# Optimization experiments

Hardware: AMD Instinct MI355X
Metric: run time of the kernel (lower is better)

## Reference

```python
import jax, jax.numpy as jnp
import numpy as np

N = 25000   # total nodes across the batch of graphs
K = 16      # sample_size_per_layer
H = 128     # encoder_hidden_dim
E = 128     # embedding_size
V = 32000   # vocab size
B = 50      # number of graphs / sql sequences
L = 128     # sql sequence length
NT = 4      # tokens per node name
NLAYERS = 3 # sample_layer_size


def _nrm(k, shape):
    return jax.random.normal(k, shape, dtype=jnp.float32) * 0.05


def setup_inputs() -> dict:
    key = jax.random.key(0)
    ks = iter(jax.random.split(key, 48))
    inp = {}
    inp["embed"] = _nrm(next(ks), (V, E))
    for d in ("seq_f", "seq_b", "node"):
        inp[d + "_Wih"] = _nrm(next(ks), (4 * H, E))
        inp[d + "_Whh"] = _nrm(next(ks), (4 * H, H))
        inp[d + "_b"] = _nrm(next(ks), (4 * H,))
    for d in ("fw", "bw"):
        inp[d + "_att0"] = _nrm(next(ks), (2, H))
        inp[d + "_attr"] = _nrm(next(ks), (NLAYERS - 1, 2, 2 * H))
        inp[d + "_Wg0"] = _nrm(next(ks), (H, H))
        inp[d + "_bg0"] = _nrm(next(ks), (H,))
        inp[d + "_Wgr"] = _nrm(next(ks), (NLAYERS - 1, 2 * H, 2 * H))
        inp[d + "_bgr"] = _nrm(next(ks), (NLAYERS - 1, 2 * H))
        inp[d + "_Wo0"] = _nrm(next(ks), (2, H, H))
        inp[d + "_bo0"] = _nrm(next(ks), (2, H))
        inp[d + "_Wor"] = _nrm(next(ks), (NLAYERS - 1, 2, 2 * H, H))
        inp[d + "_bor"] = _nrm(next(ks), (NLAYERS - 1, 2, H))
    inp["node_features"] = jax.random.randint(next(ks), (N, NT), 0, V)
    inp["fw_adj"] = jax.random.randint(next(ks), (N + 1, K), 0, N + 1)  # index N = zero-pad row
    inp["bw_adj"] = jax.random.randint(next(ks), (N + 1, K), 0, N + 1)
    inp["idx_sql_seqs"] = jax.random.randint(next(ks), (B, L), 0, V)
    lens = jax.random.randint(next(ks), (B,), 16, L + 1)
    inp["sql_seqs_lens"] = lens.at[0].set(L)  # ensure max(lens) == L like pad_packed
    inp["max_len"] = 1000  # nodes per graph (equal-size graphs)
    return inp


def _lstm(x, Wih, Whh, b):
    # x: [B, T, E] -> [B, T, H]; torch LSTM gate order i, f, g, o (bih+bhh folded into b)
    xg = jnp.einsum('bte,ge->btg', x, Wih) + b
    h0 = jnp.zeros((x.shape[0], Whh.shape[1]), x.dtype)
    def step(carry, gt):
        h, c = carry
        g = gt + h @ Whh.T
        i, f, gg, o = jnp.split(g, 4, axis=-1)
        c = jax.nn.sigmoid(f) * c + jax.nn.sigmoid(i) * jnp.tanh(gg)
        h = jax.nn.sigmoid(o) * jnp.tanh(c)
        return (h, c), h
    _, hs = jax.lax.scan(step, (h0, h0), jnp.swapaxes(xg, 0, 1))
    return jnp.swapaxes(hs, 0, 1)


def _gated_attn(self_h, neigh, att, Wg, bg, Wo, bo):
    # additive attention over K sampled neighbors, gated context, concat output (2*H)
    scores = jnp.einsum('nkd,d->nk', neigh, att[1]) + (self_h @ att[0])[:, None]
    a = jax.nn.softmax(scores, axis=-1)
    ctx = jnp.einsum('nk,nkd->nd', a, neigh)
    gate = jax.nn.sigmoid(self_h @ Wg + bg)
    from_self = jax.nn.relu(self_h @ Wo[0] + bo[0])
    from_neigh = jax.nn.relu((gate * ctx) @ Wo[1] + bo[1])
    return jnp.concatenate([from_self, from_neigh], axis=-1)


def reference(embed, seq_f_Wih, seq_f_Whh, seq_f_b, seq_b_Wih, seq_b_Whh, seq_b_b,
              node_Wih, node_Whh, node_b,
              fw_att0, fw_attr, fw_Wg0, fw_bg0, fw_Wgr, fw_bgr, fw_Wo0, fw_bo0, fw_Wor, fw_bor,
              bw_att0, bw_attr, bw_Wg0, bw_bg0, bw_Wgr, bw_bgr, bw_Wo0, bw_bo0, bw_Wor, bw_bor,
              node_features, fw_adj, bw_adj, idx_sql_seqs, sql_seqs_lens, max_len):
    Bq, Lq = idx_sql_seqs.shape
    # --- SQL sequence encoder: bi-LSTM with length-aware reverse (pack/pad semantics) ---
    se = embed[idx_sql_seqs]                              # [B, L, E]
    fwd = _lstm(se, seq_f_Wih, seq_f_Whh, seq_f_b)
    rev_idx = jnp.clip(sql_seqs_lens[:, None] - 1 - jnp.arange(Lq)[None, :], 0, Lq - 1)
    se_rev = jnp.take_along_axis(se, rev_idx[..., None], 1)
    bwd = jnp.take_along_axis(_lstm(se_rev, seq_b_Wih, seq_b_Whh, seq_b_b), rev_idx[..., None], 1)
    valid = (jnp.arange(Lq)[None, :] < sql_seqs_lens[:, None])[..., None]
    seqs_encoding = jnp.concatenate([fwd, bwd], -1) * valid  # padded positions zeroed
    seqs_encoding_mask = (idx_sql_seqs == 0)
    # --- node feature encoder: last hidden of a uni-LSTM over node tokens ---
    node_embedding = _lstm(embed[node_features], node_Wih, node_Whh, node_b)[:, -1, :]  # [N, H]
    fw_nbrs = fw_adj[:-1]  # [N, K]
    bw_nbrs = bw_adj[:-1]
    fw_hidden = node_embedding
    bw_hidden = node_embedding
    for l in range(NLAYERS):
        pad = jnp.zeros((1, fw_hidden.shape[1]), fw_hidden.dtype)
        fn = jnp.concatenate([fw_hidden, pad], 0)[fw_nbrs]  # [N, K, d]
        if l == 0:
            fw_hidden = _gated_attn(fw_hidden, fn, fw_att0, fw_Wg0, fw_bg0, fw_Wo0, fw_bo0)
        else:
            j = l - 1
            fw_hidden = _gated_attn(fw_hidden, fn, fw_attr[j], fw_Wgr[j], fw_bgr[j], fw_Wor[j], fw_bor[j])
        bn_ = jnp.concatenate([bw_hidden, pad], 0)[bw_nbrs]
        if l == 0:
            bw_hidden = _gated_attn(bw_hidden, bn_, bw_att0, bw_Wg0, bw_bg0, bw_Wo0, bw_bo0)
        else:
            j = l - 1
            bw_hidden = _gated_attn(bw_hidden, bn_, bw_attr[j], bw_Wgr[j], bw_bgr[j], bw_Wor[j], bw_bor[j])
    hidden = jax.nn.relu(jnp.concatenate([fw_hidden, bw_hidden], -1))  # [N, 4H]
    graph_hidden = hidden.reshape(hidden.shape[0] // max_len, max_len, hidden.shape[1])
    graph_embedding = graph_hidden.max(axis=1)
    return (graph_hidden, graph_embedding, max_len, seqs_encoding, seqs_encoding_mask)
```

## Files before the change

kernel.cpp:

```cpp
#include <hip/hip_runtime.h>
#include <math.h>

#define NN 25000
#define KNB 16
#define HH 128
#define VV 32000
#define BB 50
#define LL 128
#define NTK 4
#define NGRAPH 25
#define GCH 20

typedef __attribute__((ext_vector_type(8))) short s16x8;
typedef __attribute__((ext_vector_type(4))) float f32x4;
typedef _Float16 h16x2 __attribute__((ext_vector_type(2)));

__device__ __forceinline__ float fexp2(float x) {
#if __has_builtin(__builtin_amdgcn_exp2f)
    return __builtin_amdgcn_exp2f(x);
#else
    return exp2f(x);
#endif
}
__device__ __forceinline__ float frcp(float x) {
#if __has_builtin(__builtin_amdgcn_rcpf)
    return __builtin_amdgcn_rcpf(x);
#else
    return 1.f / x;
#endif
}
__device__ __forceinline__ float fsigm(float x) { return frcp(1.f + fexp2(x * -1.4426950408889634f)); }
__device__ __forceinline__ float ftanh(float x) { return 1.f - 2.f * frcp(1.f + fexp2(x * 2.8853900817779268f)); }

__device__ __forceinline__ unsigned short f2bf(float x) {
    unsigned int u = __float_as_uint(x);
    unsigned int r = (u + 0x7fffu + ((u >> 16) & 1u)) >> 16;
    return (unsigned short)r;
}
__device__ __forceinline__ float bf2f(unsigned int b) {
    return __uint_as_float((b & 0xffffu) << 16);
}

template<int CTRL>
__device__ __forceinline__ float qxor(float x) {
#if __has_builtin(__builtin_amdgcn_mov_dpp)
    return __int_as_float(__builtin_amdgcn_mov_dpp(__float_as_int(x), CTRL, 0xf, 0xf, true));
#else
    int m = (CTRL == 0xB1) ? 1 : (CTRL == 0x4E) ? 2 : 3;
    return __shfl_xor(x, m, 64);
#endif
}

__device__ __forceinline__ float hdot(unsigned int a, unsigned int b, float c) {
#if __has_builtin(__builtin_amdgcn_fdot2)
    return __builtin_amdgcn_fdot2(__builtin_bit_cast(h16x2, a), __builtin_bit_cast(h16x2, b), c, false);
#else
    h16x2 av = __builtin_bit_cast(h16x2, a), bv = __builtin_bit_cast(h16x2, b);
    return c + (float)av[0] * (float)bv[0] + (float)av[1] * (float)bv[1];
#endif
}

__global__ __launch_bounds__(256) void embconv_k(const float* __restrict__ e,
                                                 unsigned short* __restrict__ o)
{
    int i = blockIdx.x * 256 + threadIdx.x;
    if (i < VV * 128) o[i] = f2bf(e[i]);
}

__global__ __launch_bounds__(256) void wprep_k(
    const float* __restrict__ ndWih, const float* __restrict__ ndWhh,
    const float* __restrict__ fWg0, const float* __restrict__ fWgr,
    const float* __restrict__ fWo0, const float* __restrict__ fWor,
    const float* __restrict__ bWg0, const float* __restrict__ bWgr,
    const float* __restrict__ bWo0, const float* __restrict__ bWor,
    const float* __restrict__ sfWih, const float* __restrict__ sbWih,
    const float* __restrict__ sfWhh, const float* __restrict__ sbWhh,
    unsigned short* __restrict__ dst)
{
    int idx = blockIdx.x * 256 + threadIdx.x;
    if (idx >= 1146880) return;
    if (idx >= 884736) {
        int r = idx - 884736;
        int d = r >> 17;
        int o = r & 131071;
        int pairIdx = o >> 1, hf = o & 1;
        int k2 = pairIdx >> 9, n = pairIdx & 511;
        int k = k2 * 2 + hf;
        int unit = n >> 2, gate = n & 3;
        const float* W = d ? sbWhh : sfWhh;
        _Float16 hv = (_Float16)W[(gate * 128 + unit) * 128 + k];
        dst[idx] = __builtin_bit_cast(unsigned short, hv);
        return;
    }
    float val;
    if (idx < 131072) {
        int r = idx >> 8, k = idx & 255;
        int unit = r >> 2, gate = r & 3;
        int srow = (gate << 7) + unit;
        val = (k < 128) ? ndWih[srow * 128 + k] : ndWhh[srow * 128 + (k - 128)];
    } else if (idx < 753664) {
        int r = idx - 131072;
        int dir = r / 311296;
        int o = r % 311296;
        const float* Wg0 = dir ? bWg0 : fWg0;
        const float* Wgr = dir ? bWgr : fWgr;
        const float* Wo0 = dir ? bWo0 : fWo0;
        const float* Wor = dir ? bWor : fWor;
        if (o < 16384) {
            int n = o >> 7, k = o & 127;
            val = Wg0[k * 128 + n];
        } else if (o < 147456) {
            int p = o - 16384;
            int j = p >> 16, q = p & 65535;
            int n = q >> 8, k = q & 255;
            val = Wgr[j * 65536 + k * 256 + n];
        } else if (o < 180224) {
            int p = o - 147456;
            int s = p >> 14, q = p & 16383;
            int n = q >> 7, k = q & 127;
            val = Wo0[s * 16384 + k * 128 + n];
        } else {
            int p = o - 180224;
            int js = p >> 15, q = p & 32767;
            int n = q >> 8, k = q & 255;
            val = Wor[js * 32768 + k * 128 + n];
        }
    } else if (idx < 819200) {
        val = sfWih[idx - 753664];
    } else {
        val = sbWih[idx - 819200];
    }
    dst[idx] = f2bf(val);
}

__global__ __launch_bounds__(256) void tokrev_k(const int* __restrict__ idx,
                                                const int* __restrict__ lens,
                                                int* __restrict__ tokrev)
{
    int t = blockIdx.x * 256 + threadIdx.x;
    if (t >= BB * LL) return;
    int b = t / LL, tt = t % LL;
    int r = lens[b] - 1 - tt;
    r = r < 0 ? 0 : (r > LL - 1 ? LL - 1 : r);
    tokrev[t] = idx[b * LL + r];
}

__global__ __launch_bounds__(256) void hgemm1_k(
    const unsigned short* __restrict__ embedbf,
    const int* __restrict__ gidxA, const int* __restrict__ gidxB,
    const unsigned short* __restrict__ WtA, const unsigned short* __restrict__ WtB,
    const float* __restrict__ biasA, const float* __restrict__ biasB,
    float* __restrict__ outA, float* __restrict__ outB)
{
    __shared__ unsigned short Asm[128 * 64];
    __shared__ unsigned short Bsm[128 * 64];
    const int tid = threadIdx.x;
    const int lane = tid & 63, w = tid >> 6;
    const int wm = w >> 1, wn = w & 1;
    const int lane15 = lane & 15, hi = lane >> 4;
    const int y = blockIdx.y;
    const int* gidx = (y < 4) ? gidxA : gidxB;
    const unsigned short* Wt = (y < 4) ? WtA : WtB;
    const float* bias = (y < 4) ? biasA : biasB;
    float* outp = (y < 4) ? outA : outB;
    const int bm0 = blockIdx.x * 128, bn0 = (y & 3) * 128;
    const int M = BB * LL, K = 128;
    f32x4 acc[4][4];
#pragma unroll
    for (int i = 0; i < 4; ++i)
#pragma unroll
        for (int j = 0; j < 4; ++j) acc[i][j] = (f32x4){0.f, 0.f, 0.f, 0.f};

    for (int kt = 0; kt < K; kt += 64) {
#pragma unroll
        for (int r = 0; r < 4; ++r) {
            int id = tid + r * 256;
            int row = id >> 3, cc = id & 7;
            int m = bm0 + row;
            s16x8 v = {0, 0, 0, 0, 0, 0, 0, 0};
            if (m < M) {
                int g = gidx[m];
                v = *(const s16x8*)(embedbf + (size_t)g * 128 + kt + cc * 8);
            }
            int byt = (cc * 16) ^ ((row & 7) << 4);
            *(s16x8*)((char*)Asm + row * 128 + byt) = v;
        }
#pragma unroll
        for (int r = 0; r < 4; ++r) {
            int id = tid + r * 256;
            int row = id >> 3, cc = id & 7;
            s16x8 v = *(const s16x8*)(Wt + (size_t)(bn0 + row) * K + kt + cc * 8);
            int byt = (cc * 16) ^ ((row & 7) << 4);
            *(s16x8*)((char*)Bsm + row * 128 + byt) = v;
        }
        __syncthreads();
#pragma unroll
        for (int ks = 0; ks < 2; ++ks) {
            s16x8 af[4], bf[4];
#pragma unroll
            for (int mi = 0; mi < 4; ++mi) {
                int row = wm * 64 + mi * 16 + lane15;
                int byt = (ks * 64 + (hi * 16)) ^ ((row & 7) << 4);
                af[mi] = *(const s16x8*)((char*)Asm + row * 128 + byt);
            }
#pragma unroll
            for (int ni = 0; ni < 4; ++ni) {
                int row = wn * 64 + ni * 16 + lane15;
                int byt = (ks * 64 + (hi * 16)) ^ ((row & 7) << 4);
                bf[ni] = *(const s16x8*)((char*)Bsm + row * 128 + byt);
            }
#pragma unroll
            for (int mi = 0; mi < 4; ++mi)
#pragma unroll
                for (int ni = 0; ni < 4; ++ni)
                    acc[mi][ni] = __builtin_amdgcn_mfma_f32_16x16x32_bf16(af[mi], bf[ni], acc[mi][ni], 0, 0, 0);
        }
        __syncthreads();
    }
#pragma unroll
    for (int mi = 0; mi < 4; ++mi) {
#pragma unroll
        for (int ni = 0; ni < 4; ++ni) {
            int n = bn0 + wn * 64 + ni * 16 + lane15;
#pragma unroll
            for (int j = 0; j < 4; ++j) {
                int m = bm0 + wm * 64 + mi * 16 + hi * 4 + j;
                if (m < M) {
                    float v = acc[mi][ni][j] + bias[n];
                    int nn = ((n & 127) << 2) | (n >> 7);
                    outp[(size_t)m * 512 + nn] = v;
                }
            }
        }
    }
}

__global__ __launch_bounds__(512, 4) void node_seq_k(
    const unsigned short* __restrict__ embedbf,
    const int* __restrict__ nodefeat,
    const unsigned short* __restrict__ hrd,
    const unsigned short* __restrict__ nodeW,
    const float* __restrict__ ndb,
    unsigned short* __restrict__ hwr,
    unsigned short* __restrict__ cbuf,
    int step,
    const float* __restrict__ xgf, const float* __restrict__ xgb,
    const unsigned short* __restrict__ wseq,
    const int* __restrict__ lens,
    float* __restrict__ senc,
    unsigned short* __restrict__ hseq, float* __restrict__ cseq)
{
    __shared__ __align__(16) unsigned char smem[32768 + 512];
    const int bid = blockIdx.x;
    const int tid = threadIdx.x;

    if (bid >= 784) {
        int sid = bid - 784;
        int dir = sid >= BB ? 1 : 0;
        int b = dir ? sid - BB : sid;
        int len = lens[b];
        int t0 = step * 32;
        if (t0 >= len) return;
        int t1 = t0 + 32 < len ? t0 + 32 : len;
        const float* xg = (dir ? xgb : xgf) + (size_t)b * LL * 512;
        const unsigned int* wp = (const unsigned int*)(wseq + dir * 131072);
        int q = tid & 3, unit = tid >> 2;
        unsigned int wreg[64];
#pragma unroll
        for (int k2 = 0; k2 < 64; ++k2) wreg[k2] = wp[k2 * 512 + tid];
        unsigned short* hlsq = (unsigned short*)smem;
        float cj = 0.f;
        if (step == 0) {
            if (tid < 128) hlsq[tid] = 0;
        } else {
            if (tid < 128) hlsq[tid] = hseq[sid * 128 + tid];
            if (q == 0) cj = cseq[sid * 128 + unit];
        }
        __syncthreads();
        float xcur = xg[(size_t)t0 * 512 + tid];
        int pb = 0;
        for (int t = t0; t < t1; ++t) {
            float xnext = (t + 1 < t1) ? xg[(size_t)(t + 1) * 512 + tid] : 0.f;
            const uint4* hp = (const uint4*)&hlsq[pb * 128];
            float p0 = 0.f, p1 = 0.f, p2 = 0.f, p3 = 0.f;
#pragma unroll
            for (int i = 0; i < 4; ++i) {
                uint4 h0 = hp[i * 4 + 0], h1 = hp[i * 4 + 1], h2 = hp[i * 4 + 2], h3 = hp[i * 4 + 3];
                const unsigned int* w0 = &wreg[i * 16];
                p0 = hdot(h0.x, w0[0], p0);  p0 = hdot(h0.y, w0[1], p0);
                p0 = hdot(h0.z, w0[2], p0);  p0 = hdot(h0.w, w0[3], p0);
                p1 = hdot(h1.x, w0[4], p1);  p1 = hdot(h1.y, w0[5], p1);
                p1 = hdot(h1.z, w0[6], p1);  p1 = hdot(h1.w, w0[7], p1);
                p2 = hdot(h2.x, w0[8], p2);  p2 = hdot(h2.y, w0[9], p2);
                p2 = hdot(h2.z, w0[10], p2); p2 = hdot(h2.w, w0[11], p2);
                p3 = hdot(h3.x, w0[12], p3); p3 = hdot(h3.y, w0[13], p3);
                p3 = hdot(h3.z, w0[14], p3); p3 = hdot(h3.w, w0[15], p3);
            }
            float accv = xcur + ((p0 + p1) + (p2 + p3));
            float tv = (q == 2) ? ftanh(accv) : fsigm(accv);
            float v1 = __shfl_xor(tv, 1), v2 = __shfl_xor(tv, 2), v3 = __shfl_xor(tv, 3);
            if (q == 0) {
                cj = v1 * cj + tv * v2;
                float hv = v3 * ftanh(cj);
                _Float16 hh = (_Float16)hv;
                hlsq[(pb ^ 1) * 128 + unit] = __builtin_bit_cast(unsigned short, hh);
                int tout = dir ? (len - 1 - t) : t;
                senc[((size_t)b * LL + tout) * 256 + dir * 128 + unit] = hv;
            }
            __syncthreads();
            pb ^= 1;
            xcur = xnext;
        }
        if (q == 0) cseq[sid * 128 + unit] = cj;
        if (tid < 128) hseq[sid * 128 + tid] = hlsq[pb * 128 + tid];
        return;
    }

    unsigned short* Asm = (unsigned short*)smem;
    unsigned short* Bsm = (unsigned short*)(smem + 16384);
    const int lane = tid & 63, w = tid >> 6;
    const int wm = w & 1, wn = w >> 1;
    const int lane15 = lane & 15, hi = lane >> 4, q = lane & 3;
    const int bx = bid % 196, y = bid / 196;
    const int bm0 = bx * 128, bn0 = y * 128;
    const int czero = (step == 0);

    f32x4 acc[4][2];
#pragma unroll
    for (int i = 0; i < 4; ++i)
#pragma unroll
        for (int j = 0; j < 2; ++j) acc[i][j] = (f32x4){0.f, 0.f, 0.f, 0.f};

    for (int kt = 0; kt < 256; kt += 64) {
#pragma unroll
        for (int r = 0; r < 2; ++r) {
            int id = tid + r * 512;
            int row = id >> 3, cc = id & 7;
            int m = bm0 + row;
            s16x8 v = {0, 0, 0, 0, 0, 0, 0, 0};
            if (m < NN) {
                int k0 = kt + cc * 8;
                if (k0 < 128) {
                    int g = nodefeat[m * NTK + step];
                    v = *(const s16x8*)(embedbf + (size_t)g * 128 + k0);
                } else if (!czero) {
                    v = *(const s16x8*)(hrd + (size_t)m * 128 + (k0 - 128));
                }
            }
            int byt = (cc * 16) ^ ((row & 7) << 4);
            *(s16x8*)((char*)Asm + row * 128 + byt) = v;
        }
#pragma unroll
        for (int r = 0; r < 2; ++r) {
            int id = tid + r * 512;
            int row = id >> 3, cc = id & 7;
            s16x8 v = *(const s16x8*)(nodeW + (size_t)(bn0 + row) * 256 + kt + cc * 8);
            int byt = (cc * 16) ^ ((row & 7) << 4);
            *(s16x8*)((char*)Bsm + row * 128 + byt) = v;
        }
        __syncthreads();
#pragma unroll
        for (int ks = 0; ks < 2; ++ks) {
            s16x8 af[4], bf[2];
#pragma unroll
            for (int mi = 0; mi < 4; ++mi) {
                int row = wm * 64 + mi * 16 + lane15;
                int byt = (ks * 64 + (hi * 16)) ^ ((row & 7) << 4);
                af[mi] = *(const s16x8*)((char*)Asm + row * 128 + byt);
            }
#pragma unroll
            for (int ni = 0; ni < 2; ++ni) {
                int row = wn * 32 + ni * 16 + lane15;
                int byt = (ks * 64 + (hi * 16)) ^ ((row & 7) << 4);
                bf[ni] = *(const s16x8*)((char*)Bsm + row * 128 + byt);
            }
#pragma unroll
            for (int mi = 0; mi < 4; ++mi)
#pragma unroll
                for (int ni = 0; ni < 2; ++ni)
                    acc[mi][ni] = __builtin_amdgcn_mfma_f32_16x16x32_bf16(af[mi], bf[ni], acc[mi][ni], 0, 0, 0);
        }
        __syncthreads();
    }
    unsigned short* cb = cbuf + (((size_t)bid * 8 + w) * 64 + lane) * 8;
    float crv[8];
    if (czero) {
#pragma unroll
        for (int i = 0; i < 8; ++i) crv[i] = 0.f;
    } else {
        uint4 w0 = *(const uint4*)cb;
        unsigned int wd[4] = {w0.x, w0.y, w0.z, w0.w};
#pragma unroll
        for (int i = 0; i < 8; ++i) crv[i] = bf2f(wd[i >> 1] >> ((i & 1) * 16));
    }
    const bool qb0 = (lane & 1), qb1 = (lane & 2);
#pragma unroll
    for (int mi = 0; mi < 4; ++mi) {
#pragma unroll
        for (int ni = 0; ni < 2; ++ni) {
            int n = bn0 + wn * 32 + ni * 16 + lane15;
            int unit = n >> 2;
            float bval = ndb[((n & 3) << 7) + unit];
#pragma unroll
            for (int j = 0; j < 4; ++j) {
                float v = acc[mi][ni][j] + bval;
                float tv = (q == 2) ? ftanh(v) : fsigm(v);
                float v1 = qxor<0xB1>(tv), v2 = qxor<0x4E>(tv), v3 = qxor<0x1B>(tv);
                if (q == j) {
                    float gf = qb0 ? (qb1 ? v2 : tv) : (qb1 ? v3 : v1);
                    float gig = qb0 ? (v1 * v3) : (tv * v2);
                    float go = qb0 ? (qb1 ? tv : v2) : (qb1 ? v1 : v3);
                    float cc = gf * crv[mi * 2 + ni] + gig;
                    crv[mi * 2 + ni] = cc;
                    int m = bm0 + wm * 64 + mi * 16 + hi * 4 + j;
                    if (m < NN) hwr[(size_t)m * HH + unit] = f2bf(go * ftanh(cc));
                }
            }
        }
    }
    unsigned int wd[4];
#pragma unroll
    for (int p = 0; p < 4; ++p)
        wd[p] = (unsigned int)f2bf(crv[2 * p]) | ((unsigned int)f2bf(crv[2 * p + 1]) << 16);
    *(uint4*)cb = make_uint4(wd[0], wd[1], wd[2], wd[3]);
}

template<int OF32OUT>
__global__ __launch_bounds__(256) void hgemm3b_k(
    const unsigned short* __restrict__ cur, int curds,
    unsigned short* __restrict__ ctx, int ctxds,
    const unsigned short* __restrict__ wg, int wgds,
    const float* __restrict__ bgf, const float* __restrict__ bgb,
    const unsigned short* __restrict__ wo, int wods, int wrs,
    const float* __restrict__ bof, const float* __restrict__ bob,
    void* __restrict__ outb, int outds, int ocolDS,
    int M, int K, int D, int gatetiles, int roleoff)
{
    __shared__ unsigned short Asm[128 * 64];
    __shared__ unsigned short Bsm[128 * 64];
    const int tid = threadIdx.x;
    const int lane = tid & 63, w = tid >> 6;
    const int wm = w >> 1, wn = w & 1;
    const int bm0 = blockIdx.x * 128;
    const int dir = blockIdx.z, y = blockIdx.y;
    const bool isgate = y < gatetiles;
    const int r = isgate ? 0 : (y - gatetiles + roleoff);
    const int colBase = isgate ? y * 128 : r * 128;
    unsigned short* ctxd = ctx + (size_t)dir * ctxds;
    const unsigned short* A = (isgate || r == 0) ? (cur + (size_t)dir * curds) : ctxd;
    const unsigned short* Wt = isgate ? (wg + (size_t)dir * wgds + (size_t)colBase * K)
                                      : (wo + (size_t)dir * wods + (size_t)r * wrs);
    const float* bias = (isgate ? (dir ? bgb : bgf) : (dir ? bob : bof)) + colBase;

    f32x4 acc[4][4];
#pragma unroll
    for (int i = 0; i < 4; ++i)
#pragma unroll
        for (int j = 0; j < 4; ++j) acc[i][j] = (f32x4){0.f, 0.f, 0.f, 0.f};

    for (int kt = 0; kt < K; kt += 64) {
#pragma unroll
        for (int rr = 0; rr < 4; ++rr) {
            int id = tid + rr * 256;
            int row = id >> 3, cc = id & 7;
            int m = bm0 + row;
            s16x8 v = {0, 0, 0, 0, 0, 0, 0, 0};
            if (m < M) v = *(const s16x8*)(A + (size_t)m * K + kt + cc * 8);
            int byt = (cc * 16) ^ ((row & 7) << 4);
            *(s16x8*)((char*)Asm + row * 128 + byt) = v;
        }
#pragma unroll
        for (int rr = 0; rr < 4; ++rr) {
            int id = tid + rr * 256;
            int row = id >> 3, cc = id & 7;
            s16x8 v = *(const s16x8*)(Wt + (size_t)row * K + kt + cc * 8);
            int byt = (cc * 16) ^ ((row & 7) << 4);
            *(s16x8*)((char*)Bsm + row * 128 + byt) = v;
        }
        __syncthreads();
#pragma unroll
        for (int ks = 0; ks < 2; ++ks) {
            s16x8 af[4], bf[4];
#pragma unroll
            for (int mi = 0; mi < 4; ++mi) {
                int row = wm * 64 + mi * 16 + (lane & 15);
                int byt = (ks * 64 + ((lane >> 4) * 16)) ^ ((row & 7) << 4);
                af[mi] = *(const s16x8*)((char*)Asm + row * 128 + byt);
            }
#pragma unroll
            for (int ni = 0; ni < 4; ++ni) {
                int row = wn * 64 + ni * 16 + (lane & 15);
                int byt = (ks * 64 + ((lane >> 4) * 16)) ^ ((row & 7) << 4);
                bf[ni] = *(const s16x8*)((char*)Bsm + row * 128 + byt);
            }
#pragma unroll
            for (int mi = 0; mi < 4; ++mi)
#pragma unroll
                for (int ni = 0; ni < 4; ++ni)
                    acc[mi][ni] = __builtin_amdgcn_mfma_f32_16x16x32_bf16(af[mi], bf[ni], acc[mi][ni], 0, 0, 0);
        }
        __syncthreads();
    }
#pragma unroll
    for (int mi = 0; mi < 4; ++mi) {
#pragma unroll
        for (int ni = 0; ni < 4; ++ni) {
            int ncol = wn * 64 + ni * 16 + (lane & 15);
            int col = colBase + ncol;
#pragma unroll
            for (int j = 0; j < 4; ++j) {
                int m = bm0 + wm * 64 + mi * 16 + (lane >> 4) * 4 + j;
                if (m < M) {
                    float v = acc[mi][ni][j] + bias[ncol];
                    if (isgate) {
                        v = fsigm(v) * bf2f(ctxd[(size_t)m * D + col]);
                        ctxd[(size_t)m * D + col] = f2bf(v);
                    } else if (OF32OUT) {
                        v = fmaxf(v, 0.f);
                        ((float*)outb)[(size_t)m * 512 + dir * ocolDS + col] = v;
                    } else {
                        v = fmaxf(v, 0.f);
                        ((unsigned short*)outb)[(size_t)dir * outds + (size_t)m * 256 + col] = f2bf(v);
                    }
                }
            }
        }
    }
}

__global__ __launch_bounds__(256) void finalize_k(const int* __restrict__ idx,
                                                  const int* __restrict__ lens,
                                                  float* __restrict__ senc,
                                                  float* __restrict__ mask,
                                                  float* __restrict__ omax,
                                                  const int* __restrict__ mlin)
{
    int id = blockIdx.x * 256 + threadIdx.x;
    if (id == 0) omax[0] = (float)mlin[0];
    if (id >= BB * LL * 64) return;
    int row = id >> 6, c = id & 63;
    int b = row / LL, tt = row % LL;
    if (c == 0) mask[row] = (idx[row] == 0) ? 1.f : 0.f;
    if (tt >= lens[b]) *(float4*)&senc[(size_t)row * 256 + c * 4] = make_float4(0.f, 0.f, 0.f, 0.f);
}

template<int D>
__global__ __launch_bounds__(256) void sdot_k(const unsigned short* __restrict__ hidb, int hidds,
                                              const float* __restrict__ a1f, const float* __restrict__ a1b,
                                              float* __restrict__ s1)
{
    constexpr int V = D / 64;
    int dir = blockIdx.y;
    const unsigned short* hid = hidb + (size_t)dir * hidds;
    const float* att1 = dir ? a1b : a1f;
    int lane = threadIdx.x & 63, wid = threadIdx.x >> 6;
    int n = blockIdx.x * 4 + wid;
    if (n >= NN) return;
    float p = 0.f;
    if (V == 2) {
        unsigned int u = *(const unsigned int*)(hid + (size_t)n * D + lane * 2);
        p = bf2f(u) * att1[lane * 2] + bf2f(u >> 16) * att1[lane * 2 + 1];
    } else {
        uint2 u = *(const uint2*)(hid + (size_t)n * D + lane * 4);
        p = bf2f(u.x) * att1[lane * 4] + bf2f(u.x >> 16) * att1[lane * 4 + 1]
          + bf2f(u.y) * att1[lane * 4 + 2] + bf2f(u.y >> 16) * att1[lane * 4 + 3];
    }
#pragma unroll
    for (int m = 1; m < 64; m <<= 1) p += __shfl_xor(p, m);
    if (lane == 0) s1[dir * NN + n] = p;
}

template<int D>
__global__ __launch_bounds__(256) void attn_ctx3_k(const unsigned short* __restrict__ hidb, int hidds,
                                                   const int* __restrict__ adj0, const int* __restrict__ adj1,
                                                   const float* __restrict__ s1,
                                                   unsigned short* __restrict__ ctxb, int ctxds)
{
    constexpr int V = D / 64;
    int dir = blockIdx.y;
    const unsigned short* hid = hidb + (size_t)dir * hidds;
    const int* adj = dir ? adj1 : adj0;
    unsigned short* ctx = ctxb + (size_t)dir * ctxds;
    int lane = threadIdx.x & 63, wid = threadIdx.x >> 6;
    int n = blockIdx.x * 4 + wid;
    if (n >= NN) return;
    int nb[KNB];
    float sc[KNB];
#pragma unroll
    for (int k = 0; k < KNB; ++k) nb[k] = adj[n * KNB + k];
#pragma unroll
    for (int k = 0; k < KNB; ++k) sc[k] = (nb[k] < NN) ? s1[dir * NN + nb[k]] : 0.f;
    float mx = sc[0];
#pragma unroll
    for (int k = 1; k < KNB; ++k) mx = fmaxf(mx, sc[k]);
    float s = 0.f;
#pragma unroll
    for (int k = 0; k < KNB; ++k) { sc[k] = fexp2((sc[k] - mx) * 1.4426950408889634f); s += sc[k]; }
    float inv = frcp(s);
    float accv[V];
#pragma unroll
    for (int j = 0; j < V; ++j) accv[j] = 0.f;
#pragma unroll
    for (int k = 0; k < KNB; ++k) {
        if (nb[k] < NN) {
            if (V == 2) {
                unsigned int u = *(const unsigned int*)(hid + (size_t)nb[k] * D + lane * 2);
                accv[0] += sc[k] * bf2f(u);
                accv[1] += sc[k] * bf2f(u >> 16);
            } else {
                uint2 u = *(const uint2*)(hid + (size_t)nb[k] * D + lane * 4);
                accv[0] += sc[k] * bf2f(u.x);
                accv[1] += sc[k] * bf2f(u.x >> 16);
                accv[2] += sc[k] * bf2f(u.y);
                accv[3] += sc[k] * bf2f(u.y >> 16);
            }
        }
    }
#pragma unroll
    for (int j2 = 0; j2 < V; j2 += 2) {
        unsigned int pk = (unsigned int)f2bf(accv[j2] * inv) | ((unsigned int)f2bf(accv[j2 + 1] * inv) << 16);
        *(unsigned int*)(ctx + (size_t)n * D + lane * V + j2) = pk;
    }
}

__global__ __launch_bounds__(512) void gmax1_k(const float* __restrict__ gh, float* __restrict__ part)
{
    int g = blockIdx.x, ch = blockIdx.y;
    int c = threadIdx.x;
    const float* p = gh + ((size_t)g * 1000 + ch * (1000 / GCH)) * 512 + c;
    float m = -1e30f;
#pragma unroll 5
    for (int i = 0; i < 1000 / GCH; ++i) m = fmaxf(m, p[(size_t)i * 512]);
    part[((size_t)g * GCH + ch) * 512 + c] = m;
}

__global__ __launch_bounds__(512) void gmax2_k(const float* __restrict__ part, float* __restrict__ ge)
{
    int g = blockIdx.x;
    int c = threadIdx.x;
    float m = -1e30f;
#pragma unroll
    for (int i = 0; i < GCH; ++i) m = fmaxf(m, part[((size_t)g * GCH + i) * 512 + c]);
    ge[g * 512 + c] = m;
}

extern "C" void kernel_launch(void* const* d_in, const int* in_sizes, int n_in,
                              void* d_out, int out_size, void* d_ws, size_t ws_size,
                              hipStream_t stream)
{
    const float* embed = (const float*)d_in[0];
    const float* sfWhh = (const float*)d_in[2];
    const float* sfb   = (const float*)d_in[3];
    const float* sbWhh = (const float*)d_in[5];
    const float* sbb   = (const float*)d_in[6];
    const float* ndWih = (const float*)d_in[7];
    const float* ndWhh = (const float*)d_in[8];
    const float* ndb   = (const float*)d_in[9];
    const int* nodefeat = (const int*)d_in[30];
    const int* adj0     = (const int*)d_in[31];
    const int* adj1     = (const int*)d_in[32];
    const int* idxseq   = (const int*)d_in[33];
    const int* lens     = (const int*)d_in[34];
    const int* mlin     = (const int*)d_in[35];

    float* ws = (float*)d_ws;
    unsigned short* warena  = (unsigned short*)ws;
    unsigned short* embedbf = (unsigned short*)(ws + 573440);
    float* xgf = ws + 2621440;
    float* xgb = ws + 5898240;
    int*   tokrev = (int*)(ws + 9175040);
    unsigned short* hbf  = (unsigned short*)(ws + 9181440);
    unsigned short* hbf2 = (unsigned short*)(ws + 10781440);
    unsigned short* cbuf = (unsigned short*)(ws + 12381440);
    unsigned short* HA   = (unsigned short*)(ws + 573440);
    unsigned short* HB   = (unsigned short*)(ws + 6973440);
    unsigned short* ctxb = (unsigned short*)(ws + 13987072);
    float* s1buf = ws + 20387072;
    unsigned short* hseq = (unsigned short*)(ws + 20437072);
    float* cseq = ws + 20449872;
    float* gmaxp = ws + 573440;

    float* outf  = (float*)d_out;
    float* gh    = outf;
    float* ge    = outf + 12800000;
    float* omax  = outf + 12812800;
    float* senc  = outf + 12812801;
    float* omask = outf + 14451201;

    tokrev_k<<<dim3((BB * LL + 255) / 256), dim3(256), 0, stream>>>(idxseq, lens, tokrev);
    embconv_k<<<dim3(VV * 128 / 256), dim3(256), 0, stream>>>(embed, embedbf);
    wprep_k<<<dim3(4480), dim3(256), 0, stream>>>(ndWih, ndWhh,
        (const float*)d_in[12], (const float*)d_in[14], (const float*)d_in[16], (const float*)d_in[18],
        (const float*)d_in[22], (const float*)d_in[24], (const float*)d_in[26], (const float*)d_in[28],
        (const float*)d_in[1], (const float*)d_in[4], sfWhh, sbWhh, warena);

    hgemm1_k<<<dim3(50, 8), dim3(256), 0, stream>>>(embedbf, idxseq, tokrev,
        warena + 753664, warena + 819200, sfb, sbb, xgf, xgb);

    for (int t = 0; t < NTK; ++t) {
        const unsigned short* hrd = (t & 1) ? hbf2 : hbf;
        unsigned short* hwr = (t & 1) ? hbf : hbf2;
        node_seq_k<<<dim3(884), dim3(512), 0, stream>>>(embedbf, nodefeat, hrd,
            warena, ndb, hwr, cbuf, t,
            xgf, xgb, warena + 884736, lens, senc, hseq, cseq);
    }
    finalize_k<<<dim3(1600), dim3(256), 0, stream>>>(idxseq, lens, senc, omask, omax, mlin);

    for (int l = 0; l < 3; ++l) {
        int D = (l == 0) ? 128 : 256;
        int j = l - 1;
        const unsigned short* curb = (l == 0) ? hbf : (l == 1 ? HA : HB);
        int curds = (l == 0) ? 0 : NN * 256;
        int ctxds = NN * D;
        const float* a1f = (l == 0) ? (const float*)d_in[10] + 128 : (const float*)d_in[11] + (size_t)j * 512 + 256;
        const float* a1b = (l == 0) ? (const float*)d_in[20] + 128 : (const float*)d_in[21] + (size_t)j * 512 + 256;

        if (D == 128) {
            sdot_k<128><<<dim3(NN / 4, 2), dim3(256), 0, stream>>>(curb, curds, a1f, a1b, s1buf);
            attn_ctx3_k<128><<<dim3(NN / 4, 2), dim3(256), 0, stream>>>(curb, curds, adj0, adj1, s1buf, ctxb, ctxds);
        } else {
            sdot_k<256><<<dim3(NN / 4, 2), dim3(256), 0, stream>>>(curb, curds, a1f, a1b, s1buf);
            attn_ctx3_k<256><<<dim3(NN / 4, 2), dim3(256), 0, stream>>>(curb, curds, adj0, adj1, s1buf, ctxb, ctxds);
        }

        const unsigned short* wgb = warena + 131072 + ((l == 0) ? 0 : 16384 + j * 65536);
        const float* bgf = (l == 0) ? (const float*)d_in[13] : (const float*)d_in[15] + (size_t)j * 256;
        const float* bgb = (l == 0) ? (const float*)d_in[23] : (const float*)d_in[25] + (size_t)j * 256;
        const unsigned short* wob = warena + 131072 + ((l == 0) ? 147456 : 180224 + j * 65536);
        int wrs = (l == 0) ? 16384 : 32768;
        const float* bof = (l == 0) ? (const float*)d_in[17] : (const float*)d_in[19] + (size_t)j * 256;
        const float* bob = (l == 0) ? (const float*)d_in[27] : (const float*)d_in[29] + (size_t)j * 256;
        int gt = D / 128;
        void* ob = (l == 2) ? (void*)gh : (void*)((l == 0) ? HA : HB);
        int outds = NN * 256;

        if (l == 2) {
            hgemm3b_k<1><<<dim3(196, gt + 1, 2), dim3(256), 0, stream>>>(curb, curds, ctxb, ctxds,
                wgb, 311296, bgf, bgb, wob, 311296, wrs, bof, bob, ob, 0, 256, NN, D, D, gt, 0);
            hgemm3b_k<1><<<dim3(196, 1, 2), dim3(256), 0, stream>>>(curb, curds, ctxb, ctxds,
                wgb, 311296, bgf, bgb, wob, 311296, wrs, bof, bob, ob, 0, 256, NN, D, D, 0, 1);
        } else {
            hgemm3b_k<0><<<dim3(196, gt + 1, 2), dim3(256), 0, stream>>>(curb, curds, ctxb, ctxds,
                wgb, 311296, bgf, bgb, wob, 311296, wrs, bof, bob, ob, outds, 0, NN, D, D, gt, 0);
            hgemm3b_k<0><<<dim3(196, 1, 2), dim3(256), 0, stream>>>(curb, curds, ctxb, ctxds,
                wgb, 311296, bgf, bgb, wob, 311296, wrs, bof, bob, ob, outds, 0, NN, D, D, 0, 1);
        }
    }

    gmax1_k<<<dim3(NGRAPH, GCH), dim3(512), 0, stream>>>(gh, gmaxp);
    gmax2_k<<<dim3(NGRAPH), dim3(512), 0, stream>>>(gmaxp, ge);
}
```

Baseline: 653.9 us.

## Fuse gate and output GEMMs per layer into one kernel keeping activations in LDS

Replaces the two hgemm3b launches per layer with a single layer_fused_k kernel. Each block loads its 128-row tile of the current hidden state into shared memory once, computes the gate GEMMs and writes the gated context into shared memory instead of global, then runs both output GEMMs from LDS. This removes the global round trip for the gated context, the repeated A-tile loads and one launch per layer, and swizzles the block index so the two directions are spread across the grid. In exchange it uses large LDS allocations (up to about 144KB at D=256) with one 512-thread block per CU, which limits occupancy, and the grid is only 392 blocks.

Result: faster. 606.2 us (median of 5 runs) (-7.3%).

```diff
diff --git a/kernel.cpp b/kernel.cpp
--- a/kernel.cpp
+++ b/kernel.cpp
@@ -425,102 +425,166 @@
     *(uint4*)cb = make_uint4(wd[0], wd[1], wd[2], wd[3]);
 }
 
-template<int OF32OUT>
-__global__ __launch_bounds__(256) void hgemm3b_k(
+template<int D, int OF32OUT>
+__global__ __launch_bounds__(512, 1) void layer_fused_k(
     const unsigned short* __restrict__ cur, int curds,
-    unsigned short* __restrict__ ctx, int ctxds,
+    const unsigned short* __restrict__ ctx, int ctxds,
     const unsigned short* __restrict__ wg, int wgds,
     const float* __restrict__ bgf, const float* __restrict__ bgb,
     const unsigned short* __restrict__ wo, int wods, int wrs,
     const float* __restrict__ bof, const float* __restrict__ bob,
-    void* __restrict__ outb, int outds, int ocolDS,
-    int M, int K, int D, int gatetiles, int roleoff)
-{
-    __shared__ unsigned short Asm[128 * 64];
-    __shared__ unsigned short Bsm[128 * 64];
+    void* __restrict__ outb, int outds)
+{
+    __shared__ unsigned short As[128 * D];
+    __shared__ unsigned short Gs[128 * D];
+    __shared__ unsigned short Ws[128 * 64];
+    constexpr int gt = D / 128;
     const int tid = threadIdx.x;
     const int lane = tid & 63, w = tid >> 6;
-    const int wm = w >> 1, wn = w & 1;
-    const int bm0 = blockIdx.x * 128;
-    const int dir = blockIdx.z, y = blockIdx.y;
-    const bool isgate = y < gatetiles;
-    const int r = isgate ? 0 : (y - gatetiles + roleoff);
-    const int colBase = isgate ? y * 128 : r * 128;
-    unsigned short* ctxd = ctx + (size_t)dir * ctxds;
-    const unsigned short* A = (isgate || r == 0) ? (cur + (size_t)dir * curds) : ctxd;
-    const unsigned short* Wt = isgate ? (wg + (size_t)dir * wgds + (size_t)colBase * K)
-                                      : (wo + (size_t)dir * wods + (size_t)r * wrs);
-    const float* bias = (isgate ? (dir ? bgb : bgf) : (dir ? bob : bof)) + colBase;
-
-    f32x4 acc[4][4];
-#pragma unroll
-    for (int i = 0; i < 4; ++i)
-#pragma unroll
-        for (int j = 0; j < 4; ++j) acc[i][j] = (f32x4){0.f, 0.f, 0.f, 0.f};
-
-    for (int kt = 0; kt < K; kt += 64) {
-#pragma unroll
-        for (int rr = 0; rr < 4; ++rr) {
-            int id = tid + rr * 256;
-            int row = id >> 3, cc = id & 7;
-            int m = bm0 + row;
-            s16x8 v = {0, 0, 0, 0, 0, 0, 0, 0};
-            if (m < M) v = *(const s16x8*)(A + (size_t)m * K + kt + cc * 8);
-            int byt = (cc * 16) ^ ((row & 7) << 4);
-            *(s16x8*)((char*)Asm + row * 128 + byt) = v;
-        }
-#pragma unroll
-        for (int rr = 0; rr < 4; ++rr) {
-            int id = tid + rr * 256;
-            int row = id >> 3, cc = id & 7;
-            s16x8 v = *(const s16x8*)(Wt + (size_t)row * K + kt + cc * 8);
-            int byt = (cc * 16) ^ ((row & 7) << 4);
-            *(s16x8*)((char*)Bsm + row * 128 + byt) = v;
-        }
-        __syncthreads();
-#pragma unroll
-        for (int ks = 0; ks < 2; ++ks) {
-            s16x8 af[4], bf[4];
-#pragma unroll
-            for (int mi = 0; mi < 4; ++mi) {
-                int row = wm * 64 + mi * 16 + (lane & 15);
-                int byt = (ks * 64 + ((lane >> 4) * 16)) ^ ((row & 7) << 4);
-                af[mi] = *(const s16x8*)((char*)Asm + row * 128 + byt);
-            }
-#pragma unroll
-            for (int ni = 0; ni < 4; ++ni) {
-                int row = wn * 64 + ni * 16 + (lane & 15);
-                int byt = (ks * 64 + ((lane >> 4) * 16)) ^ ((row & 7) << 4);
-                bf[ni] = *(const s16x8*)((char*)Bsm + row * 128 + byt);
-            }
-#pragma unroll
-            for (int mi = 0; mi < 4; ++mi)
-#pragma unroll
-                for (int ni = 0; ni < 4; ++ni)
-                    acc[mi][ni] = __builtin_amdgcn_mfma_f32_16x16x32_bf16(af[mi], bf[ni], acc[mi][ni], 0, 0, 0);
-        }
-        __syncthreads();
-    }
-#pragma unroll
-    for (int mi = 0; mi < 4; ++mi) {
-#pragma unroll
-        for (int ni = 0; ni < 4; ++ni) {
-            int ncol = wn * 64 + ni * 16 + (lane & 15);
-            int col = colBase + ncol;
-#pragma unroll
-            for (int j = 0; j < 4; ++j) {
-                int m = bm0 + wm * 64 + mi * 16 + (lane >> 4) * 4 + j;
-                if (m < M) {
-                    float v = acc[mi][ni][j] + bias[ncol];
+    const int wm = w & 1, wn = w >> 1;
+    const int lane15 = lane & 15, hi = lane >> 4;
+    const int orig = blockIdx.x;
+    const int work = (orig & 7) * 49 + (orig >> 3);
+    const int dir = work / 196;
+    const int mt = work % 196;
+    const int bm0 = mt * 128;
+    const unsigned short* curd = cur + (size_t)dir * curds;
+    const unsigned short* ctxd = ctx + (size_t)dir * ctxds;
+    const float* bg = dir ? bgb : bgf;
+    const float* bo = dir ? bob : bof;
+
+    constexpr int CH = D / 8;
+#pragma unroll
+    for (int r = 0; r < D / 32; ++r) {
+        int id = tid + r * 512;
+        int row = id / CH, cc = id % CH;
+        int m = bm0 + row;
+        s16x8 v = {0, 0, 0, 0, 0, 0, 0, 0};
+        if (m < NN) v = *(const s16x8*)(curd + (size_t)m * D + cc * 8);
+        *(s16x8*)((char*)As + row * (D * 2) + ((cc * 16) ^ ((row & 7) << 4))) = v;
+    }
+    __syncthreads();
+
+#pragma unroll
+    for (int p = 0; p <= gt; ++p) {
+        const bool isgate = p < gt;
+        const int colBase = isgate ? p * 128 : 0;
+        const unsigned short* Wt = isgate ? (wg + (size_t)dir * wgds + (size_t)colBase * D)
+                                          : (wo + (size_t)dir * wods);
+        f32x4 acc[4][2];
+#pragma unroll
+        for (int i = 0; i < 4; ++i)
+#pragma unroll
+            for (int j = 0; j < 2; ++j) acc[i][j] = (f32x4){0.f, 0.f, 0.f, 0.f};
+        for (int kt = 0; kt < D; kt += 64) {
+#pragma unroll
+            for (int r = 0; r < 2; ++r) {
+                int id = tid + r * 512;
+                int row = id >> 3, cc = id & 7;
+                s16x8 v = *(const s16x8*)(Wt + (size_t)row * D + kt + cc * 8);
+                *(s16x8*)((char*)Ws + row * 128 + ((cc * 16) ^ ((row & 7) << 4))) = v;
+            }
+            __syncthreads();
+#pragma unroll
+            for (int ks = 0; ks < 2; ++ks) {
+                s16x8 af[4], bf[2];
+#pragma unroll
+                for (int mi = 0; mi < 4; ++mi) {
+                    int row = wm * 64 + mi * 16 + lane15;
+                    af[mi] = *(const s16x8*)((char*)As + row * (D * 2)
+                              + (((kt + ks * 32 + hi * 8) * 2) ^ ((row & 7) << 4)));
+                }
+#pragma unroll
+                for (int ni = 0; ni < 2; ++ni) {
+                    int row = wn * 32 + ni * 16 + lane15;
+                    bf[ni] = *(const s16x8*)((char*)Ws + row * 128
+                              + (((ks * 32 + hi * 8) * 2) ^ ((row & 7) << 4)));
+                }
+#pragma unroll
+                for (int mi = 0; mi < 4; ++mi)
+#pragma unroll
+                    for (int ni = 0; ni < 2; ++ni)
+                        acc[mi][ni] = __builtin_amdgcn_mfma_f32_16x16x32_bf16(af[mi], bf[ni], acc[mi][ni], 0, 0, 0);
+            }
+            __syncthreads();
+        }
+#pragma unroll
+        for (int mi = 0; mi < 4; ++mi) {
+#pragma unroll
+            for (int ni = 0; ni < 2; ++ni) {
+                int ncol = wn * 32 + ni * 16 + lane15;
+#pragma unroll
+                for (int j = 0; j < 4; ++j) {
+                    int rr = wm * 64 + mi * 16 + hi * 4 + j;
+                    int m = bm0 + rr;
                     if (isgate) {
-                        v = fsigm(v) * bf2f(ctxd[(size_t)m * D + col]);
-                        ctxd[(size_t)m * D + col] = f2bf(v);
-                    } else if (OF32OUT) {
-                        v = fmaxf(v, 0.f);
-                        ((float*)outb)[(size_t)m * 512 + dir * ocolDS + col] = v;
-                    } else {
-                        v = fmaxf(v, 0.f);
-                        ((unsigned short*)outb)[(size_t)dir * outds + (size_t)m * 256 + col] = f2bf(v);
+                        int col = colBase + ncol;
+                        float v = acc[mi][ni][j] + bg[col];
+                        int ma = (m < NN) ? m : 0;
+                        v = fsigm(v) * bf2f(ctxd[(size_t)ma * D + col]);
+                        *(unsigned short*)((char*)Gs + rr * (D * 2) + ((col * 2) ^ ((rr & 7) << 4))) = f2bf(v);
+                    } else if (m < NN) {
+                        float v = fmaxf(acc[mi][ni][j] + bo[ncol], 0.f);
+                        if (OF32OUT) ((float*)outb)[(size_t)m * 512 + dir * 256 + ncol] = v;
+                        else ((unsigned short*)outb)[(size_t)dir * outds + (size_t)m * 256 + ncol] = f2bf(v);
+                    }
+                }
+            }
+        }
+    }
+    __syncthreads();
+
+    {
+        const unsigned short* Wt = wo + (size_t)dir * wods + (size_t)wrs;
+        f32x4 acc[4][2];
+#pragma unroll
+        for (int i = 0; i < 4; ++i)
+#pragma unroll
+            for (int j = 0; j < 2; ++j) acc[i][j] = (f32x4){0.f, 0.f, 0.f, 0.f};
+        for (int kt = 0; kt < D; kt += 64) {
+#pragma unroll
+            for (int r = 0; r < 2; ++r) {
+                int id = tid + r * 512;
+                int row = id >> 3, cc = id & 7;
+                s16x8 v = *(const s16x8*)(Wt + (size_t)row * D + kt + cc * 8);
+                *(s16x8*)((char*)Ws + row * 128 + ((cc * 16) ^ ((row & 7) << 4))) = v;
+            }
+            __syncthreads();
+#pragma unroll
+            for (int ks = 0; ks < 2; ++ks) {
+                s16x8 af[4], bf[2];
+#pragma unroll
+                for (int mi = 0; mi < 4; ++mi) {
+                    int row = wm * 64 + mi * 16 + lane15;
+                    af[mi] = *(const s16x8*)((char*)Gs + row * (D * 2)
+                              + (((kt + ks * 32 + hi * 8) * 2) ^ ((row & 7) << 4)));
+                }
+#pragma unroll
+                for (int ni = 0; ni < 2; ++ni) {
+                    int row = wn * 32 + ni * 16 + lane15;
+                    bf[ni] = *(const s16x8*)((char*)Ws + row * 128
+                              + (((ks * 32 + hi * 8) * 2) ^ ((row & 7) << 4)));
+                }
+#pragma unroll
+                for (int mi = 0; mi < 4; ++mi)
+#pragma unroll
+                    for (int ni = 0; ni < 2; ++ni)
+                        acc[mi][ni] = __builtin_amdgcn_mfma_f32_16x16x32_bf16(af[mi], bf[ni], acc[mi][ni], 0, 0, 0);
+            }
+            __syncthreads();
+        }
+#pragma unroll
+        for (int mi = 0; mi < 4; ++mi) {
+#pragma unroll
+            for (int ni = 0; ni < 2; ++ni) {
+                int ncol = wn * 32 + ni * 16 + lane15;
+#pragma unroll
+                for (int j = 0; j < 4; ++j) {
+                    int m = bm0 + wm * 64 + mi * 16 + hi * 4 + j;
+                    if (m < NN) {
+                        float v = fmaxf(acc[mi][ni][j] + bo[128 + ncol], 0.f);
+                        if (OF32OUT) ((float*)outb)[(size_t)m * 512 + dir * 256 + 128 + ncol] = v;
+                        else ((unsigned short*)outb)[(size_t)dir * outds + (size_t)m * 256 + 128 + ncol] = f2bf(v);
                     }
                 }
             }
@@ -730,20 +794,17 @@
         int wrs = (l == 0) ? 16384 : 32768;
         const float* bof = (l == 0) ? (const float*)d_in[17] : (const float*)d_in[19] + (size_t)j * 256;
         const float* bob = (l == 0) ? (const float*)d_in[27] : (const float*)d_in[29] + (size_t)j * 256;
-        int gt = D / 128;
-        void* ob = (l == 2) ? (void*)gh : (void*)((l == 0) ? HA : HB);
         int outds = NN * 256;
 
-        if (l == 2) {
-            hgemm3b_k<1><<<dim3(196, gt + 1, 2), dim3(256), 0, stream>>>(curb, curds, ctxb, ctxds,
-                wgb, 311296, bgf, bgb, wob, 311296, wrs, bof, bob, ob, 0, 256, NN, D, D, gt, 0);
-            hgemm3b_k<1><<<dim3(196, 1, 2), dim3(256), 0, stream>>>(curb, curds, ctxb, ctxds,
-                wgb, 311296, bgf, bgb, wob, 311296, wrs, bof, bob, ob, 0, 256, NN, D, D, 0, 1);
+        if (l == 0) {
+            layer_fused_k<128, 0><<<dim3(392), dim3(512), 0, stream>>>(curb, curds, ctxb, ctxds,
+                wgb, 311296, bgf, bgb, wob, 311296, wrs, bof, bob, HA, outds);
+        } else if (l == 1) {
+            layer_fused_k<256, 0><<<dim3(392), dim3(512), 0, stream>>>(curb, curds, ctxb, ctxds,
+                wgb, 311296, bgf, bgb, wob, 311296, wrs, bof, bob, HB, outds);
         } else {
-            hgemm3b_k<0><<<dim3(196, gt + 1, 2), dim3(256), 0, stream>>>(curb, curds, ctxb, ctxds,
-                wgb, 311296, bgf, bgb, wob, 311296, wrs, bof, bob, ob, outds, 0, NN, D, D, gt, 0);
-            hgemm3b_k<0><<<dim3(196, 1, 2), dim3(256), 0, stream>>>(curb, curds, ctxb, ctxds,
-                wgb, 311296, bgf, bgb, wob, 311296, wrs, bof, bob, ob, outds, 0, NN, D, D, 0, 1);
+            layer_fused_k<256, 1><<<dim3(392), dim3(512), 0, stream>>>(curb, curds, ctxb, ctxds,
+                wgb, 311296, bgf, bgb, wob, 311296, wrs, bof, bob, gh, 0);
         }
     }
 
```
